# Performance work log

Measured on AMD Instinct MI355X. Metric: run time of the kernel, lower is better.

Reference implementation:

```python
import jax, jax.numpy as jnp
import numpy as np

N_QUBITS = 9   # kernelsize**2
N_LAYERS = 2   # BasicEntanglerLayers depth
KS = 3
FILTERS = 4


def _rx(theta):
    # RX(theta) = [[cos(t/2), -i sin(t/2)], [-i sin(t/2), cos(t/2)]]
    c = jnp.cos(theta / 2).astype(jnp.complex64)
    s = (-1j) * jnp.sin(theta / 2).astype(jnp.complex64)
    return jnp.stack([jnp.stack([c, s]), jnp.stack([s, c])])


def _apply_1q(state, gate, wire):
    # state: (2,)*N_QUBITS complex64
    s = jnp.moveaxis(state, wire, 0).reshape(2, -1)
    s = gate @ s
    return jnp.moveaxis(s.reshape((2,) * N_QUBITS), 0, wire)


def _apply_cnot(state, c, t):
    s0 = jnp.take(state, 0, axis=c)
    s1 = jnp.take(state, 1, axis=c)
    ft = t if t < c else t - 1  # target axis index after removing control axis
    s1 = jnp.flip(s1, axis=ft)
    return jnp.stack([s0, s1], axis=c)


def _circuit(p, w):
    # p: (N_QUBITS,) input angles; w: (N_LAYERS, N_QUBITS) trainable angles
    state = jnp.zeros((2,) * N_QUBITS, dtype=jnp.complex64).at[(0,) * N_QUBITS].set(1.0)
    # AngleEmbedding (rotation='X', PennyLane default)
    for i in range(N_QUBITS):
        state = _apply_1q(state, _rx(p[i]), i)
    # BasicEntanglerLayers: RX rotations + CNOT ring per layer
    for l in range(N_LAYERS):
        for i in range(N_QUBITS):
            state = _apply_1q(state, _rx(w[l, i]), i)
        for i in range(N_QUBITS):
            state = _apply_cnot(state, i, (i + 1) % N_QUBITS)
    probs = state.real ** 2 + state.imag ** 2
    z = []
    for i in range(N_QUBITS):
        pi = probs.sum(axis=tuple(a for a in range(N_QUBITS) if a != i))  # (2,)
        z.append(pi[0] - pi[1])  # <Z_i>
    return jnp.stack(z)  # (N_QUBITS,)


def setup_inputs() -> dict:
    key = jax.random.key(0)
    k1, k2 = jax.random.split(key)
    x = jax.random.normal(k1, (4, 3, 28, 28), dtype=jnp.float32)
    qweights = jax.random.uniform(k2, (N_LAYERS, N_QUBITS), dtype=jnp.float32, minval=0.0, maxval=2.0 * np.pi)
    return {"x": x, "qweights": qweights}


def reference(x, qweights):
    B, C, H, W = x.shape
    h_out = H - KS + 1
    w_out = W - KS + 1
    # Patch extraction: (B, C, h_out, w_out, KS*KS)
    patches = jnp.stack(
        [x[:, :, dy:dy + h_out, dx:dx + w_out] for dy in range(KS) for dx in range(KS)],
        axis=-1,
    )
    # With stride=1 the overlapping scatter writes in the original are fully
    # overwritten by later iterations, so out[b,f,y,x,c] == circuit(patch)[f].
    q = jax.vmap(_circuit, in_axes=(0, None))(patches.reshape(-1, KS * KS), qweights)
    q = q.reshape(B, C, h_out, w_out, N_QUBITS)[..., :FILTERS]
    out = q.mean(axis=1)  # mean over channels -> (B, h_out, w_out, F)
    return jnp.transpose(out, (0, 3, 1, 2))  # (B, F, h_out, w_out)
```

## Files before the change

kernel.cpp:

```cpp
#include <hip/hip_runtime.h>


static constexpr int BQ = 4;
static constexpr int CH = 3;
static constexpr int HOUT = 26;
static constexpr int WOUT = 26;

__device__ __forceinline__ float shflx(float v, int m) {
  return __shfl_xor(v, m, 64);
}

__global__ __launch_bounds__(192) void quanv_kernel(
    const float* __restrict__ x,
    const float* __restrict__ w,
    float* __restrict__ out)
{
  __shared__ float sm[CH * 4];

  const int pix  = blockIdx.x;
  const int b    = pix / (HOUT * WOUT);
  const int r    = pix % (HOUT * WOUT);
  const int oy   = r / WOUT;
  const int ox   = r % WOUT;
  const int ch   = threadIdx.x >> 6;
  const int lane = threadIdx.x & 63;

  float ci[9], si[9];
#pragma unroll
  for (int i = 0; i < 9; ++i) {
    const int dy = i / 3, dx = i % 3;
    const float p  = x[((b * CH + ch) * 28 + (oy + dy)) * 28 + (ox + dx)];
    const float th = 0.5f * (p + w[i]);
    ci[i] = __cosf(th);
    si[i] = __sinf(th);
  }
  float c1[9], s1[9];
#pragma unroll
  for (int q = 0; q < 9; ++q) {
    const float th = 0.5f * w[9 + q];
    c1[q] = __cosf(th);
    s1[q] = __sinf(th);
  }

  float plo = 1.f;
#pragma unroll
  for (int q = 0; q < 6; ++q)
    plo *= ((lane >> q) & 1) ? si[q] : ci[q];
  const int pclo = __popc(lane);

  float tr[8], ti[8];
#pragma unroll
  for (int k = 0; k < 8; ++k) {
    const float r8 = plo * ((k & 1) ? si[6] : ci[6])
                         * ((k & 2) ? si[7] : ci[7])
                         * ((k & 4) ? si[8] : ci[8]);
    const int pc = (pclo + __popc(k)) & 3;
    tr[k] = (pc == 0) ? r8 : ((pc == 2) ? -r8 : 0.f);
    ti[k] = (pc == 3) ? r8 : ((pc == 1) ? -r8 : 0.f);
  }

  constexpr int LXm[9] = {3, 6, 12, 24, 48, 32, 0, 0, 3};
  constexpr int KXm[9] = {0, 0, 0,  0,  0,  1,  3, 6, 4};
#pragma unroll
  for (int q = 0; q < 9; ++q) {
    const float c = c1[q], s = s1[q];
    float pr[8], pim[8];
#pragma unroll
    for (int k = 0; k < 8; ++k) {
      float vr = tr[k ^ KXm[q]];
      float vi = ti[k ^ KXm[q]];
      if (LXm[q] != 0) {
        vr = shflx(vr, LXm[q]);
        vi = shflx(vi, LXm[q]);
      }
      pr[k] = vr;
      pim[k] = vi;
    }
#pragma unroll
    for (int k = 0; k < 8; ++k) {
      const float ntr = c * tr[k] + s * pim[k];
      const float nti = c * ti[k] - s * pr[k];
      tr[k] = ntr;
      ti[k] = nti;
    }
  }

  float prob[8];
#pragma unroll
  for (int k = 0; k < 8; ++k) prob[k] = tr[k] * tr[k] + ti[k] * ti[k];

  constexpr int ROW[4] = {0x154, 0x1FD, 0x1FA, 0x1F5};
  float z[4];
#pragma unroll
  for (int f = 0; f < 4; ++f) {
    const int hi = ROW[f] >> 6;
    const int lo = ROW[f] & 63;
    float acc = 0.f;
#pragma unroll
    for (int k = 0; k < 8; ++k)
      acc += (__popc(hi & k) & 1) ? -prob[k] : prob[k];
    z[f] = (__popc(lo & lane) & 1) ? -acc : acc;
  }

#pragma unroll
  for (int m = 1; m < 64; m <<= 1) {
#pragma unroll
    for (int f = 0; f < 4; ++f) z[f] += shflx(z[f], m);
  }
  if (lane == 0) {
#pragma unroll
    for (int f = 0; f < 4; ++f) sm[ch * 4 + f] = z[f];
  }
  __syncthreads();

  if (threadIdx.x < 4) {
    const int f = threadIdx.x;
    const float v = (sm[f] + sm[4 + f] + sm[8 + f]) * (1.f / 3.f);
    out[((b * 4 + f) * HOUT + oy) * WOUT + ox] = v;
  }
}

extern "C" void kernel_launch(void* const* d_in, const int* in_sizes, int n_in,
                              void* d_out, int out_size, void* d_ws, size_t ws_size,
                              hipStream_t stream) {
  const float* x = (const float*)d_in[0];
  const float* w = (const float*)d_in[1];
  float* out = (float*)d_out;
  dim3 grid(BQ * HOUT * WOUT);
  dim3 block(192);
  hipLaunchKernelGGL(quanv_kernel, grid, block, 0, stream, x, w, out);
}
```

Before: 67.34 us.

## Relabel state basis so layer-2 rotations use cheaper lane/register pairings

Changes the basis labelling of the statevector (lane index is mapped through a Gray-code-like transform jl) so that the second-layer RX gates pair amplitudes at single-bit lane distances or within registers. This lets some rotations happen fully in-register without shuffles, and pairs others to share a shuffle. The Z-expectation masks are recomputed for the new basis. It also computes sin/cos inline to shorten live ranges and adds a min-blocks hint to launch_bounds. The risk is correctness of the remapped masks and register pressure under the occupancy hint.

```diff
diff --git a/kernel.cpp b/kernel.cpp
--- a/kernel.cpp
+++ b/kernel.cpp
@@ -1,7 +1,6 @@
 #include <hip/hip_runtime.h>
 
 
-static constexpr int BQ = 4;
 static constexpr int CH = 3;
 static constexpr int HOUT = 26;
 static constexpr int WOUT = 26;
@@ -10,7 +9,7 @@
   return __shfl_xor(v, m, 64);
 }
 
-__global__ __launch_bounds__(192) void quanv_kernel(
+__global__ __launch_bounds__(192, 8) void quanv_kernel(
     const float* __restrict__ x,
     const float* __restrict__ w,
     float* __restrict__ out)
@@ -24,89 +23,109 @@
   const int ox   = r % WOUT;
   const int ch   = threadIdx.x >> 6;
   const int lane = threadIdx.x & 63;
+  const int jl   = (lane ^ (lane << 1)) & 63;
 
-  float ci[9], si[9];
-#pragma unroll
-  for (int i = 0; i < 9; ++i) {
-    const int dy = i / 3, dx = i % 3;
-    const float p  = x[((b * CH + ch) * 28 + (oy + dy)) * 28 + (ox + dx)];
-    const float th = 0.5f * (p + w[i]);
-    ci[i] = __cosf(th);
-    si[i] = __sinf(th);
-  }
-  float c1[9], s1[9];
-#pragma unroll
-  for (int q = 0; q < 9; ++q) {
-    const float th = 0.5f * w[9 + q];
-    c1[q] = __cosf(th);
-    s1[q] = __sinf(th);
-  }
+  const float* xp = x + ((b * CH + ch) * 28 + oy) * 28 + ox;
 
   float plo = 1.f;
 #pragma unroll
-  for (int q = 0; q < 6; ++q)
-    plo *= ((lane >> q) & 1) ? si[q] : ci[q];
-  const int pclo = __popc(lane);
+  for (int q = 0; q < 6; ++q) {
+    const float p  = xp[(q / 3) * 28 + (q % 3)];
+    const float th = 0.5f * (p + w[q]);
+    const float c = __cosf(th), s = __sinf(th);
+    plo *= ((jl >> q) & 1) ? s : c;
+  }
+  float c6, s6, c7, s7, c8, s8;
+  { const float th = 0.5f * (xp[2 * 28 + 0] + w[6]); c6 = __cosf(th); s6 = __sinf(th); }
+  { const float th = 0.5f * (xp[2 * 28 + 1] + w[7]); c7 = __cosf(th); s7 = __sinf(th); }
+  { const float th = 0.5f * (xp[2 * 28 + 2] + w[8]); c8 = __cosf(th); s8 = __sinf(th); }
 
+  const int pclo = __popc(jl);
   float tr[8], ti[8];
 #pragma unroll
   for (int k = 0; k < 8; ++k) {
-    const float r8 = plo * ((k & 1) ? si[6] : ci[6])
-                         * ((k & 2) ? si[7] : ci[7])
-                         * ((k & 4) ? si[8] : ci[8]);
+    const float a = plo * ((k & 1) ? s6 : c6)
+                        * ((k & 2) ? s7 : c7)
+                        * ((k & 4) ? s8 : c8);
     const int pc = (pclo + __popc(k)) & 3;
-    tr[k] = (pc == 0) ? r8 : ((pc == 2) ? -r8 : 0.f);
-    ti[k] = (pc == 3) ? r8 : ((pc == 1) ? -r8 : 0.f);
+    tr[k] = (pc == 0) ? a : ((pc == 2) ? -a : 0.f);
+    ti[k] = (pc == 3) ? a : ((pc == 1) ? -a : 0.f);
   }
 
-  constexpr int LXm[9] = {3, 6, 12, 24, 48, 32, 0, 0, 3};
-  constexpr int KXm[9] = {0, 0, 0,  0,  0,  1,  3, 6, 4};
 #pragma unroll
-  for (int q = 0; q < 9; ++q) {
-    const float c = c1[q], s = s1[q];
-    float pr[8], pim[8];
+  for (int q = 0; q < 5; ++q) {
+    const float th = 0.5f * w[9 + q];
+    const float c = __cosf(th), s = __sinf(th);
+    const int Lm = 1 << q;
 #pragma unroll
     for (int k = 0; k < 8; ++k) {
-      float vr = tr[k ^ KXm[q]];
-      float vi = ti[k ^ KXm[q]];
-      if (LXm[q] != 0) {
-        vr = shflx(vr, LXm[q]);
-        vi = shflx(vi, LXm[q]);
-      }
-      pr[k] = vr;
-      pim[k] = vi;
+      const float vr = shflx(tr[k], Lm);
+      const float vi = shflx(ti[k], Lm);
+      tr[k] = c * tr[k] + s * vi;
+      ti[k] = c * ti[k] - s * vr;
     }
+  }
+  {
+    const float th = 0.5f * w[14];
+    const float c = __cosf(th), s = __sinf(th);
+#pragma unroll
+    for (int k = 0; k < 8; k += 2) {
+      const int p = k + 1;
+      const float ar = shflx(tr[p], 32), ai = shflx(ti[p], 32);
+      const float br = shflx(tr[k], 32), bi = shflx(ti[k], 32);
+      tr[k] = c * tr[k] + s * ai;  ti[k] = c * ti[k] - s * ar;
+      tr[p] = c * tr[p] + s * bi;  ti[p] = c * ti[p] - s * br;
+    }
+  }
+#pragma unroll
+  for (int qq = 0; qq < 2; ++qq) {
+    const int K = qq ? 6 : 3;
+    const float th = 0.5f * w[15 + qq];
+    const float c = __cosf(th), s = __sinf(th);
 #pragma unroll
     for (int k = 0; k < 8; ++k) {
-      const float ntr = c * tr[k] + s * pim[k];
-      const float nti = c * ti[k] - s * pr[k];
-      tr[k] = ntr;
-      ti[k] = nti;
+      const int p = k ^ K;
+      if (k < p) {
+        const float ar = tr[p], ai = ti[p];
+        const float br = tr[k], bi = ti[k];
+        tr[k] = c * br + s * ai;  ti[k] = c * bi - s * ar;
+        tr[p] = c * ar + s * bi;  ti[p] = c * ai - s * br;
+      }
+    }
+  }
+  {
+    const float th = 0.5f * w[17];
+    const float c = __cosf(th), s = __sinf(th);
+#pragma unroll
+    for (int k = 0; k < 4; ++k) {
+      const int p = k + 4;
+      const float ar = shflx(tr[p], 1), ai = shflx(ti[p], 1);
+      const float br = shflx(tr[k], 1), bi = shflx(ti[k], 1);
+      tr[k] = c * tr[k] + s * ai;  ti[k] = c * ti[k] - s * ar;
+      tr[p] = c * tr[p] + s * bi;  ti[p] = c * ti[p] - s * br;
     }
   }
 
-  float prob[8];
 #pragma unroll
-  for (int k = 0; k < 8; ++k) prob[k] = tr[k] * tr[k] + ti[k] * ti[k];
+  for (int k = 0; k < 8; ++k) tr[k] = tr[k] * tr[k] + ti[k] * ti[k];
 
-  constexpr int ROW[4] = {0x154, 0x1FD, 0x1FA, 0x1F5};
+  constexpr int RL[4] = {0x1E, 0x23, 0x27, 0x2F};
+  constexpr int RH[4] = {5, 7, 7, 7};
   float z[4];
 #pragma unroll
   for (int f = 0; f < 4; ++f) {
-    const int hi = ROW[f] >> 6;
-    const int lo = ROW[f] & 63;
     float acc = 0.f;
 #pragma unroll
     for (int k = 0; k < 8; ++k)
-      acc += (__popc(hi & k) & 1) ? -prob[k] : prob[k];
-    z[f] = (__popc(lo & lane) & 1) ? -acc : acc;
+      acc += (__popc(RH[f] & k) & 1) ? -tr[k] : tr[k];
+    z[f] = (__popc(RL[f] & lane) & 1) ? -acc : acc;
   }
 
 #pragma unroll
-  for (int m = 1; m < 64; m <<= 1) {
+  for (int m = 1; m < 64; m <<= 1)
 #pragma unroll
     for (int f = 0; f < 4; ++f) z[f] += shflx(z[f], m);
-  }
+
   if (lane == 0) {
 #pragma unroll
     for (int f = 0; f < 4; ++f) sm[ch * 4 + f] = z[f];
@@ -115,8 +134,8 @@
 
   if (threadIdx.x < 4) {
     const int f = threadIdx.x;
-    const float v = (sm[f] + sm[4 + f] + sm[8 + f]) * (1.f / 3.f);
-    out[((b * 4 + f) * HOUT + oy) * WOUT + ox] = v;
+    out[((b * 4 + f) * HOUT + oy) * WOUT + ox] =
+        (sm[f] + sm[4 + f] + sm[8 + f]) * (1.f / 3.f);
   }
 }
 
@@ -126,7 +145,7 @@
   const float* x = (const float*)d_in[0];
   const float* w = (const float*)d_in[1];
   float* out = (float*)d_out;
-  dim3 grid(BQ * HOUT * WOUT);
+  dim3 grid(4 * HOUT * WOUT);
   dim3 block(192);
   hipLaunchKernelGGL(quanv_kernel, grid, block, 0, stream, x, w, out);
 }
```

After: 68.10 us. About the same (+1.1%).
